# Kernel tuning notes

Hardware: AMD Instinct MI355X
Metric: run time of the kernel (lower is better)

## Reference

```python
import jax, jax.numpy as jnp
import numpy as np

B, C, M = 2048, 1, 80  # M = max_object; matrices are (M+1)x(M+1)


def setup_inputs() -> dict:
    key = jax.random.key(0)
    k1, k2, k3, k4 = jax.random.split(key, 4)
    inp = {
        "input": jax.random.normal(k1, (B, C, M + 1, M + 1), dtype=jnp.float32),
        "target": jax.random.randint(k2, (B, C, M + 1, M + 1), 0, 2, dtype=jnp.int32),
        "mask0": jax.random.randint(k3, (B, C, M + 1), 0, 2, dtype=jnp.int32),
        "mask1": jax.random.randint(k4, (B, C, M + 1), 0, 2, dtype=jnp.int32),
        "outputs": 0,
        "current_fair_labels": 0,
        "next_fair_labels": 0,
    }
    return inp


def reference(input, target, mask0, mask1, outputs, current_fair_labels, next_fair_labels):
    f32 = jnp.float32
    m0 = mask0.astype(f32)[:, :, :, None]   # [B,C,M+1,1] (row mask, broadcast over cols)
    m1 = mask1.astype(f32)[:, :, None, :]   # [B,C,1,M+1] (col mask, broadcast over rows)
    mask_region = m0 * m1                    # [B,C,M+1,M+1]
    mask_region_pre = mask_region.at[:, :, M, :].set(0.0)   # zero last row
    mask_region_next = mask_region.at[:, :, :, M].set(0.0)  # zero last col
    mask_region_union = mask_region_pre * mask_region_next

    input_pre = jax.nn.softmax(mask_region_pre * input, axis=3)
    input_next = jax.nn.softmax(mask_region_next * input, axis=2)
    input_all = input_pre.at[:, :, :M, :M].set(
        jnp.maximum(input_pre, input_next)[:, :, :M, :M])

    t = target.astype(jnp.bool_).astype(f32)
    target_pre = mask_region_pre * t
    target_next = mask_region_next * t
    target_union = mask_region_union * t

    target_num = t.sum()
    n_pre = target_pre.sum()
    n_next = target_next.sum()
    n_union = target_union.sum()

    s_pre = -(target_pre * jnp.log(input_pre)).sum()
    loss_pre = jnp.where(n_pre > 0, s_pre / n_pre, s_pre)

    s_next = -(target_next * jnp.log(input_next)).sum()
    loss_next = jnp.where(n_next > 0, s_next / n_next, s_next)

    s_all = -(target_pre * jnp.log(input_all)).sum()
    loss = jnp.where((n_pre > 0) & (n_next > 0), s_all / n_pre, s_all)

    # |1 - p_pre - (1 - p_next)| == |p_next - p_pre|
    s_sim = (target_union * jnp.abs(input_next - input_pre)).sum()
    loss_similarity = jnp.where(n_union > 0, s_sim / target_num, s_sim)

    # accuracy on "pre" direction (argmax over cols, drop last row)
    idx_t_pre = jnp.argmax(target_pre, axis=3)[:, :, :-1]
    indexes_pre = jnp.argmax(input_all, axis=3)[:, :, :-1]
    mpre = mask0.astype(f32)[:, :, :-1]
    n_mpre = mpre.sum()
    s_acc_pre = ((indexes_pre == idx_t_pre).astype(f32) * mpre).sum()
    accuracy_pre = jnp.where(n_mpre > 0, s_acc_pre / n_mpre, s_acc_pre + 1.0)

    # accuracy on "next" direction (argmax over rows, drop last col)
    idx_t_next = jnp.argmax(target_next, axis=2)[:, :, :-1]
    indexes_next = jnp.argmax(input_next, axis=2)[:, :, :-1]
    mnext = mask1.astype(f32)[:, :, :-1]
    n_mnext = mnext.sum()
    s_acc_next = ((indexes_next == idx_t_next).astype(f32) * mnext).sum()
    accuracy_next = jnp.where(n_mnext > 0, s_acc_next / n_mnext, s_acc_next + 1.0)

    total = (loss_pre + loss_next + loss + loss_similarity) / 4.0
    return (loss_pre, loss_next, loss_similarity, total,
            accuracy_pre, accuracy_next, (accuracy_pre + accuracy_next) / 2.0,
            indexes_pre)
```

## Files before the change

kernel.cpp:

```cpp
#include <hip/hip_runtime.h>

#define M1 81
#define MSZ 80
#define NEL (M1 * M1)
#define NTW ((NEL + 31) / 32)
#define NACC 12
#define BIGKC 1.0e30f


__global__ __launch_bounds__(512, 8) void sst_main(
    const float* __restrict__ input,
    const int* __restrict__ target,
    const int* __restrict__ mask0,
    const int* __restrict__ mask1,
    float* __restrict__ out_idx,
    float* __restrict__ part,
    int slices)
{
    __shared__ float s_x[NEL];
    __shared__ unsigned s_tb[NTW];
    __shared__ float s_m0[M1], s_m1[M1];
    __shared__ float s_kc[M1];
    __shared__ float s_invc[M1];
    __shared__ float s_pA[486];
    __shared__ float s_pC[480];
    __shared__ float s_pV[486];
    __shared__ unsigned char s_pI[486];
    __shared__ unsigned char s_pT[486];
    __shared__ unsigned s_m1w[4];
    __shared__ float s_wv[8][NACC];

    const int tid   = threadIdx.x;
    const int lane  = tid & 63;
    const int w     = tid >> 6;
    const int slice = blockIdx.x;
    const size_t base = (size_t)slice * NEL;

    if (tid < M1) s_m0[tid] = (float)mask0[slice * M1 + tid];
    else if (tid >= 128 && tid < 128 + M1) s_m1[tid - 128] = (float)mask1[slice * M1 + (tid - 128)];

    float a[NACC];
#pragma unroll
    for (int k = 0; k < NACC; ++k) a[k] = 0.0f;

    for (int i = tid; i < NEL; i += 512) {
        s_x[i] = input[base + i];
        unsigned long long m = __ballot(target[base + i] != 0);
        if (lane == 0) {
            const int w2 = (i >> 5) & ~1;
            s_tb[w2] = (unsigned)m;
            if (w2 + 1 < NTW) s_tb[w2 + 1] = (unsigned)(m >> 32);
        }
    }
    __syncthreads();

    if (w == 0) {
        const unsigned long long m = __ballot(s_m1[lane] != 0.0f);
        if (lane == 0) { s_m1w[0] = (unsigned)m; s_m1w[1] = (unsigned)(m >> 32); }
    } else if (w == 1) {
        float v = 0.0f;
        if (lane < 17) v = s_m1[64 + lane];
        const unsigned long long m = __ballot(v != 0.0f);
        if (lane == 0) { s_m1w[2] = (unsigned)m; s_m1w[3] = 0u; }
    }

    if (tid < 486) {
        const int c = tid / 6, j = tid - 6 * (tid / 6);
        const int r0 = j * 13 + ((j < 3) ? j : 3);
        const int len = (j < 3) ? 14 : 13;
        const float m1c = s_m1[c];
        const float mcol = (c == MSZ) ? 0.0f : m1c;
        float cs = 0.0f, bv = -1.0f;
        int bi = r0, ct = 127;
        for (int i = 0; i < len; ++i) {
            const int r = r0 + i;
            const int idx = r * M1 + c;
            const float m0r = s_m0[r];
            const float z = m1c * m0r * s_x[idx];
            const float e = __expf(z);
            s_x[idx] = e;
            cs += e;
            if (e > bv) { bv = e; bi = r; }
            const unsigned tb = (s_tb[idx >> 5] >> (idx & 31)) & 1u;
            if (ct == 127 && tb != 0u && (mcol * m0r) != 0.0f) ct = r;
        }
        s_pA[tid] = cs; s_pV[tid] = bv;
        s_pI[tid] = (unsigned char)bi; s_pT[tid] = (unsigned char)ct;
    }
    __syncthreads();

    if (tid < 480) {
        const int r = tid / 6, j = tid - 6 * (tid / 6);
        const int c0 = j * 13 + ((j < 3) ? j : 3);
        const int len = (j < 3) ? 14 : 13;
        const int rb = r * M1 + c0;
        float rs = 0.0f;
        for (int i = 0; i < len; ++i) rs += s_x[rb + i];
        s_pC[tid] = rs;
    } else {
        const int u = tid - 480;
        for (int c = u; c < M1; c += 32) {
            if (c < MSZ) {
                const int b = 6 * c;
                float cs = 0.0f;
#pragma unroll
                for (int k = 0; k < 6; ++k) cs += s_pA[b + k];
                float bv = s_pV[b]; int bi = s_pI[b];
#pragma unroll
                for (int k = 1; k < 6; ++k) {
                    const float v = s_pV[b + k];
                    if (v > bv) { bv = v; bi = s_pI[b + k]; }
                }
                int ct = 127;
#pragma unroll
                for (int k = 0; k < 6; ++k) ct = min(ct, (int)s_pT[b + k]);
                if (ct == 127) ct = 0;
                s_kc[c] = __logf(cs);
                s_invc[c] = 1.0f / cs;
                const float m1c = s_m1[c];
                a[9]  += (bi == ct) ? m1c : 0.0f;
                a[11] += m1c;
            } else {
                s_kc[c] = BIGKC;
                s_invc[c] = 0.0f;
            }
        }
        float tn = 0.0f;
        for (int wd = u; wd < NTW; wd += 32) tn += (float)__popc(s_tb[wd]);
        a[0] += tn;
    }
    __syncthreads();

    if (tid < 480) {
        const int r = tid / 6, j = tid - 6 * (tid / 6);
        const int c0 = j * 13 + ((j < 3) ? j : 3);
        const int len = (j < 3) ? 14 : 13;
        const int rb = r * M1;
        const int pb = 6 * r;
        const float rs = s_pC[pb] + s_pC[pb + 1] + s_pC[pb + 2]
                       + s_pC[pb + 3] + s_pC[pb + 4] + s_pC[pb + 5];
        const float lr = __logf(rs), invr = 1.0f / rs;
        const float m0f = s_m0[r];

        const int bp = rb + c0;
        const unsigned long long tw64 =
            ((unsigned long long)s_tb[(bp >> 5) + 1] << 32) | s_tb[bp >> 5];
        const int mp0 = c0 >> 5;
        const unsigned long long mw64 =
            ((unsigned long long)s_m1w[mp0 + 1] << 32) | s_m1w[mp0];
        const unsigned lenmask = (1u << len) - 1u;
        unsigned wb = (unsigned)(tw64 >> (bp & 31)) & (unsigned)(mw64 >> (c0 & 31)) & lenmask;
        if (m0f == 0.0f) wb = 0u;

        const unsigned w3 = (j == 5) ? (wb & 0x0FFFu) : wb;
        a[1] += (float)__popc(wb);
        a[2] += (float)__popc(w3);
        a[3] += (float)__popc(w3);
        const int ti = wb ? (c0 + __ffs(wb) - 1) : 127;

        float bv = -3.402823466e38f; int bi = c0;
        for (int i = 0; i < len; ++i) {
            const int c = c0 + i;
            const float val = s_x[rb + c] * fmaxf(invr, s_invc[c]);
            if (val > bv) { bv = val; bi = c; }
        }
        unsigned wl = wb;
        while (wl) {
            const int b = __ffs(wl) - 1; wl &= wl - 1u;
            const int c = c0 + b;
            const float e = s_x[rb + c];
            const float z = __logf(e);
            const float kc = s_kc[c];
            a[4] += lr - z;
            a[6] += fminf(lr, kc) - z;
            const bool c80 = (c == MSZ);
            a[5] += c80 ? 0.0f : (kc - z);
            const float es = c80 ? 0.0f : e;
            a[7] = fmaf(es, fabsf(s_invc[c] - invr), a[7]);
        }
        s_pV[tid] = bv; s_pI[tid] = (unsigned char)bi; s_pT[tid] = (unsigned char)ti;
    } else if (tid < 486) {
        const int j = tid - 480;
        const int c0 = j * 13 + ((j < 3) ? j : 3);
        const int len = (j < 3) ? 14 : 13;
        const int rb = MSZ * M1;
        const float m80 = s_m0[MSZ];
        const int bp = rb + c0;
        const unsigned long long tw64 =
            ((unsigned long long)s_tb[(bp >> 5) + 1] << 32) | s_tb[bp >> 5];
        const int mp0 = c0 >> 5;
        const unsigned long long mw64 =
            ((unsigned long long)s_m1w[mp0 + 1] << 32) | s_m1w[mp0];
        const unsigned lenmask = (1u << len) - 1u;
        unsigned wb = (unsigned)(tw64 >> (bp & 31)) & (unsigned)(mw64 >> (c0 & 31)) & lenmask;
        if (m80 == 0.0f) wb = 0u;
        if (j == 5) wb &= 0x0FFFu;
        a[2] += (float)__popc(wb);
        while (wb) {
            const int b = __ffs(wb) - 1; wb &= wb - 1u;
            const int c = c0 + b;
            a[5] += s_kc[c] - __logf(s_x[rb + c]);
        }
    }
    __syncthreads();

    if (tid < MSZ) {
        const int b = 6 * tid;
        float bv = s_pV[b]; int bi = s_pI[b];
#pragma unroll
        for (int k = 1; k < 6; ++k) {
            const float v = s_pV[b + k];
            if (v > bv) { bv = v; bi = s_pI[b + k]; }
        }
        int ti = 127;
#pragma unroll
        for (int k = 0; k < 6; ++k) ti = min(ti, (int)s_pT[b + k]);
        if (ti == 127) ti = 0;
        out_idx[(size_t)slice * MSZ + tid] = (float)bi;
        const float m0f = s_m0[tid];
        a[8]  += (bi == ti) ? m0f : 0.0f;
        a[10] += m0f;
    }

#pragma unroll
    for (int k = 0; k < NACC; ++k) {
        float v = a[k];
        for (int off = 32; off > 0; off >>= 1) v += __shfl_down(v, off);
        if (lane == 0) s_wv[w][k] = v;
    }
    __syncthreads();
    if (tid < NACC) {
        float s = 0.0f;
#pragma unroll
        for (int ww = 0; ww < 8; ++ww) s += s_wv[ww][tid];
        part[(size_t)tid * slices + slice] = s;
    }
}

__global__ __launch_bounds__(256) void sst_final(
    const float* __restrict__ part, int slices, float* __restrict__ out)
{
    __shared__ double s_part[4][NACC];
    const int tid = threadIdx.x;
    double l[NACC];
#pragma unroll
    for (int k = 0; k < NACC; ++k) l[k] = 0.0;
    for (int s = tid; s < slices; s += 256) {
#pragma unroll
        for (int k = 0; k < NACC; ++k) l[k] += (double)part[(size_t)k * slices + s];
    }
#pragma unroll
    for (int k = 0; k < NACC; ++k) {
        double v = l[k];
        for (int off = 32; off > 0; off >>= 1) v += __shfl_down(v, off);
        if ((tid & 63) == 0) s_part[tid >> 6][k] = v;
    }
    __syncthreads();
    if (tid == 0) {
        double g[NACC];
#pragma unroll
        for (int k = 0; k < NACC; ++k)
            g[k] = s_part[0][k] + s_part[1][k] + s_part[2][k] + s_part[3][k];
        const double tnum = g[0], npre = g[1], nnext = g[2], nunion = g[3];
        const double spre = g[4], snext = g[5], sall = g[6], ssim = g[7];
        const double accp = g[8], accn = g[9], nmp = g[10], nmn = g[11];
        const double loss_pre  = (npre > 0.0) ? spre / npre : spre;
        const double loss_next = (nnext > 0.0) ? snext / nnext : snext;
        const double loss      = (npre > 0.0 && nnext > 0.0) ? sall / npre : sall;
        const double loss_sim  = (nunion > 0.0) ? ssim / tnum : ssim;
        const double total = (loss_pre + loss_next + loss + loss_sim) * 0.25;
        const double ap = (nmp > 0.0) ? accp / nmp : accp + 1.0;
        const double an = (nmn > 0.0) ? accn / nmn : accn + 1.0;
        out[0] = (float)loss_pre;
        out[1] = (float)loss_next;
        out[2] = (float)loss_sim;
        out[3] = (float)total;
        out[4] = (float)ap;
        out[5] = (float)an;
        out[6] = (float)((ap + an) * 0.5);
    }
}

extern "C" void kernel_launch(void* const* d_in, const int* in_sizes, int n_in,
                              void* d_out, int out_size, void* d_ws, size_t ws_size,
                              hipStream_t stream) {
    const float* input  = (const float*)d_in[0];
    const int*   target = (const int*)d_in[1];
    const int*   mask0  = (const int*)d_in[2];
    const int*   mask1  = (const int*)d_in[3];
    float* out = (float*)d_out;
    float* part = (float*)d_ws;

    const int slices = in_sizes[0] / NEL;

    sst_main<<<slices, 512, 0, stream>>>(input, target, mask0, mask1, out + 7, part, slices);
    sst_final<<<1, 256, 0, stream>>>(part, slices, out);
}
```

Measured before the change: 168.6 us.

## Pad shared tile rows and vectorize row-pass reads with float4 column constants

Stores the 81x81 slice in shared memory with a padded row stride of 84, so each row is 16-byte aligned and row segments can be read as float4. The row passes now split columns into five 16-wide chunks plus a special-case thread for column 80. Per-column log-sum and reciprocal are packed into one float2 array so they can be fetched together. The intent is fewer LDS instructions and simpler indexing in the row reductions and argmax, at the cost of more index bookkeeping in the load loop, a different thread-to-work mapping, and separate handling for the last column.

```diff
diff --git a/kernel.cpp b/kernel.cpp
--- a/kernel.cpp
+++ b/kernel.cpp
@@ -2,6 +2,7 @@
 
 #define M1 81
 #define MSZ 80
+#define STR 84
 #define NEL (M1 * M1)
 #define NTW ((NEL + 31) / 32)
 #define NACC 12
@@ -17,13 +18,12 @@
     float* __restrict__ part,
     int slices)
 {
-    __shared__ float s_x[NEL];
+    __shared__ __align__(16) float s_x[M1 * STR];
     __shared__ unsigned s_tb[NTW];
     __shared__ float s_m0[M1], s_m1[M1];
-    __shared__ float s_kc[M1];
-    __shared__ float s_invc[M1];
+    __shared__ __align__(16) float2 s_colc[M1 + 1];
     __shared__ float s_pA[486];
-    __shared__ float s_pC[480];
+    __shared__ float s_pC[400];
     __shared__ float s_pV[486];
     __shared__ unsigned char s_pI[486];
     __shared__ unsigned char s_pT[486];
@@ -43,13 +43,19 @@
 #pragma unroll
     for (int k = 0; k < NACC; ++k) a[k] = 0.0f;
 
-    for (int i = tid; i < NEL; i += 512) {
-        s_x[i] = input[base + i];
-        unsigned long long m = __ballot(target[base + i] != 0);
-        if (lane == 0) {
-            const int w2 = (i >> 5) & ~1;
-            s_tb[w2] = (unsigned)m;
-            if (w2 + 1 < NTW) s_tb[w2 + 1] = (unsigned)(m >> 32);
+    {
+        int rs0 = tid / M1;
+        int cs0 = tid - rs0 * M1;
+        for (int i = tid; i < NEL; i += 512) {
+            s_x[rs0 * STR + cs0] = input[base + i];
+            unsigned long long m = __ballot(target[base + i] != 0);
+            if (lane == 0) {
+                const int w2 = (i >> 5) & ~1;
+                s_tb[w2] = (unsigned)m;
+                if (w2 + 1 < NTW) s_tb[w2 + 1] = (unsigned)(m >> 32);
+            }
+            rs0 += 6; cs0 += 26;
+            if (cs0 >= M1) { cs0 -= M1; rs0 += 1; }
         }
     }
     __syncthreads();
@@ -74,14 +80,15 @@
         int bi = r0, ct = 127;
         for (int i = 0; i < len; ++i) {
             const int r = r0 + i;
-            const int idx = r * M1 + c;
             const float m0r = s_m0[r];
-            const float z = m1c * m0r * s_x[idx];
+            const int ix = r * STR + c;
+            const float z = m1c * m0r * s_x[ix];
             const float e = __expf(z);
-            s_x[idx] = e;
+            s_x[ix] = e;
             cs += e;
             if (e > bv) { bv = e; bi = r; }
-            const unsigned tb = (s_tb[idx >> 5] >> (idx & 31)) & 1u;
+            const int ib = r * M1 + c;
+            const unsigned tb = (s_tb[ib >> 5] >> (ib & 31)) & 1u;
             if (ct == 127 && tb != 0u && (mcol * m0r) != 0.0f) ct = r;
         }
         s_pA[tid] = cs; s_pV[tid] = bv;
@@ -91,12 +98,14 @@
 
     if (tid < 480) {
         const int r = tid / 6, j = tid - 6 * (tid / 6);
-        const int c0 = j * 13 + ((j < 3) ? j : 3);
-        const int len = (j < 3) ? 14 : 13;
-        const int rb = r * M1 + c0;
-        float rs = 0.0f;
-        for (int i = 0; i < len; ++i) rs += s_x[rb + i];
-        s_pC[tid] = rs;
+        if (j < 5) {
+            const float4* xr = (const float4*)&s_x[r * STR + 16 * j];
+            const float4 q0 = xr[0], q1 = xr[1], q2 = xr[2], q3 = xr[3];
+            s_pC[r * 5 + j] = ((q0.x + q0.y) + (q0.z + q0.w))
+                            + ((q1.x + q1.y) + (q1.z + q1.w))
+                            + ((q2.x + q2.y) + (q2.z + q2.w))
+                            + ((q3.x + q3.y) + (q3.z + q3.w));
+        }
     } else {
         const int u = tid - 480;
         for (int c = u; c < M1; c += 32) {
@@ -115,14 +124,12 @@
 #pragma unroll
                 for (int k = 0; k < 6; ++k) ct = min(ct, (int)s_pT[b + k]);
                 if (ct == 127) ct = 0;
-                s_kc[c] = __logf(cs);
-                s_invc[c] = 1.0f / cs;
+                s_colc[c] = make_float2(__logf(cs), 1.0f / cs);
                 const float m1c = s_m1[c];
                 a[9]  += (bi == ct) ? m1c : 0.0f;
                 a[11] += m1c;
             } else {
-                s_kc[c] = BIGKC;
-                s_invc[c] = 0.0f;
+                s_colc[c] = make_float2(BIGKC, 0.0f);
             }
         }
         float tn = 0.0f;
@@ -133,59 +140,79 @@
 
     if (tid < 480) {
         const int r = tid / 6, j = tid - 6 * (tid / 6);
-        const int c0 = j * 13 + ((j < 3) ? j : 3);
-        const int len = (j < 3) ? 14 : 13;
-        const int rb = r * M1;
-        const int pb = 6 * r;
-        const float rs = s_pC[pb] + s_pC[pb + 1] + s_pC[pb + 2]
-                       + s_pC[pb + 3] + s_pC[pb + 4] + s_pC[pb + 5];
+        const int rb = r * STR;
+        const int p5 = r * 5;
+        const float e80 = s_x[rb + MSZ];
+        const float rs = s_pC[p5] + s_pC[p5 + 1] + s_pC[p5 + 2]
+                       + s_pC[p5 + 3] + s_pC[p5 + 4] + e80;
         const float lr = __logf(rs), invr = 1.0f / rs;
         const float m0f = s_m0[r];
 
-        const int bp = rb + c0;
-        const unsigned long long tw64 =
-            ((unsigned long long)s_tb[(bp >> 5) + 1] << 32) | s_tb[bp >> 5];
-        const int mp0 = c0 >> 5;
-        const unsigned long long mw64 =
-            ((unsigned long long)s_m1w[mp0 + 1] << 32) | s_m1w[mp0];
-        const unsigned lenmask = (1u << len) - 1u;
-        unsigned wb = (unsigned)(tw64 >> (bp & 31)) & (unsigned)(mw64 >> (c0 & 31)) & lenmask;
-        if (m0f == 0.0f) wb = 0u;
-
-        const unsigned w3 = (j == 5) ? (wb & 0x0FFFu) : wb;
-        a[1] += (float)__popc(wb);
-        a[2] += (float)__popc(w3);
-        a[3] += (float)__popc(w3);
-        const int ti = wb ? (c0 + __ffs(wb) - 1) : 127;
-
-        float bv = -3.402823466e38f; int bi = c0;
-        for (int i = 0; i < len; ++i) {
-            const int c = c0 + i;
-            const float val = s_x[rb + c] * fmaxf(invr, s_invc[c]);
-            if (val > bv) { bv = val; bi = c; }
-        }
-        unsigned wl = wb;
-        while (wl) {
-            const int b = __ffs(wl) - 1; wl &= wl - 1u;
-            const int c = c0 + b;
-            const float e = s_x[rb + c];
-            const float z = __logf(e);
-            const float kc = s_kc[c];
-            a[4] += lr - z;
-            a[6] += fminf(lr, kc) - z;
-            const bool c80 = (c == MSZ);
-            a[5] += c80 ? 0.0f : (kc - z);
-            const float es = c80 ? 0.0f : e;
-            a[7] = fmaf(es, fabsf(s_invc[c] - invr), a[7]);
+        float bv; int bi, ti;
+        if (j < 5) {
+            const int c0 = 16 * j;
+            const int bp = r * M1 + c0;
+            const unsigned long long tw64 =
+                ((unsigned long long)s_tb[(bp >> 5) + 1] << 32) | s_tb[bp >> 5];
+            const int mp0 = c0 >> 5;
+            const unsigned long long mw64 =
+                ((unsigned long long)s_m1w[mp0 + 1] << 32) | s_m1w[mp0];
+            unsigned wb = (unsigned)(tw64 >> (bp & 31)) & (unsigned)(mw64 >> (c0 & 31)) & 0xFFFFu;
+            if (m0f == 0.0f) wb = 0u;
+            const float pc = (float)__popc(wb);
+            a[1] += pc; a[2] += pc; a[3] += pc;
+            ti = wb ? (c0 + __ffs(wb) - 1) : 127;
+
+            const float4* xr = (const float4*)&s_x[rb + c0];
+            const float4 q0 = xr[0], q1 = xr[1], q2 = xr[2], q3 = xr[3];
+            float xe[16];
+            xe[0]=q0.x; xe[1]=q0.y; xe[2]=q0.z; xe[3]=q0.w;
+            xe[4]=q1.x; xe[5]=q1.y; xe[6]=q1.z; xe[7]=q1.w;
+            xe[8]=q2.x; xe[9]=q2.y; xe[10]=q2.z; xe[11]=q2.w;
+            xe[12]=q3.x; xe[13]=q3.y; xe[14]=q3.z; xe[15]=q3.w;
+            const float4* cp = (const float4*)&s_colc[c0];
+            bv = -3.402823466e38f; bi = c0;
+#pragma unroll
+            for (int h = 0; h < 8; ++h) {
+                const float4 cc = cp[h];
+                const float v0 = xe[2 * h]     * fmaxf(invr, cc.y);
+                if (v0 > bv) { bv = v0; bi = c0 + 2 * h; }
+                const float v1 = xe[2 * h + 1] * fmaxf(invr, cc.w);
+                if (v1 > bv) { bv = v1; bi = c0 + 2 * h + 1; }
+            }
+            unsigned wl = wb;
+            while (wl) {
+                const int b = __ffs(wl) - 1; wl &= wl - 1u;
+                const int c = c0 + b;
+                const float e = s_x[rb + c];
+                const float z = __logf(e);
+                const float2 cc2 = s_colc[c];
+                a[4] += lr - z;
+                a[5] += cc2.x - z;
+                a[6] += fminf(lr, cc2.x) - z;
+                a[7] = fmaf(e, fabsf(cc2.y - invr), a[7]);
+            }
+        } else {
+            bv = e80 * invr; bi = MSZ;
+            const int ib = r * M1 + MSZ;
+            const unsigned tb = (s_tb[ib >> 5] >> (ib & 31)) & 1u;
+            const unsigned m1b = (s_m1w[2] >> 16) & 1u;
+            const unsigned wb80 = tb & m1b & ((m0f != 0.0f) ? 1u : 0u);
+            ti = wb80 ? MSZ : 127;
+            if (wb80) {
+                const float z = __logf(e80);
+                a[1] += 1.0f;
+                a[4] += lr - z;
+                a[6] += lr - z;
+            }
         }
         s_pV[tid] = bv; s_pI[tid] = (unsigned char)bi; s_pT[tid] = (unsigned char)ti;
     } else if (tid < 486) {
         const int j = tid - 480;
         const int c0 = j * 13 + ((j < 3) ? j : 3);
         const int len = (j < 3) ? 14 : 13;
-        const int rb = MSZ * M1;
         const float m80 = s_m0[MSZ];
-        const int bp = rb + c0;
+        const int bp = MSZ * M1 + c0;
         const unsigned long long tw64 =
             ((unsigned long long)s_tb[(bp >> 5) + 1] << 32) | s_tb[bp >> 5];
         const int mp0 = c0 >> 5;
@@ -199,7 +226,7 @@
         while (wb) {
             const int b = __ffs(wb) - 1; wb &= wb - 1u;
             const int c = c0 + b;
-            a[5] += s_kc[c] - __logf(s_x[rb + c]);
+            a[5] += s_colc[c].x - __logf(s_x[MSZ * STR + c]);
         }
     }
     __syncthreads();
```

Result: no change. 171.6 us (+1.8%).
